# Performance work log

Hardware: AMD Instinct MI355X
Metric: run time of the kernel (lower is better)

Reference implementation:

```python
import jax, jax.numpy as jnp
import numpy as np

NUM_HEADS = 16


def setup_inputs() -> dict:
    key = jax.random.key(0)
    k1, k2, k3 = jax.random.split(key, 3)
    T, B, E = 2048, 2, 1024
    query = jax.random.normal(k1, (T, B, E), dtype=jnp.float32)
    # xavier-uniform-ish init for qkv weight, small normal for output proj
    lim = (6.0 / (3 * E + E)) ** 0.5
    W_qkv = jax.random.uniform(k2, (3 * E, E), dtype=jnp.float32, minval=-lim, maxval=lim)
    W_o = jax.random.normal(k3, (E, E), dtype=jnp.float32) * 0.02
    b_qkv = jnp.zeros((3 * E,), dtype=jnp.float32)
    b_o = jnp.zeros((E,), dtype=jnp.float32)
    return {"query": query, "W_qkv": W_qkv, "b_qkv": b_qkv, "W_o": W_o, "b_o": b_o}


def reference(query, W_qkv, b_qkv, W_o, b_o):
    T, B, E = query.shape
    H = NUM_HEADS
    hd = E // H
    scaling = float(hd) ** -0.5

    # fused qkv projection: [T, B, 3E]
    qkv = jnp.einsum('tbe,fe->tbf', query, W_qkv) + b_qkv
    q, k, v = jnp.split(qkv, 3, axis=-1)
    q = q * scaling

    def to_heads(x):  # [T, B, E] -> [B*H, T, hd]
        return x.reshape(T, B * H, hd).transpose(1, 0, 2)

    q, k, v = to_heads(q), to_heads(k), to_heads(v)

    # explicit bmm QK^T -> softmax -> bmm AV (faithful to source)
    scores = jnp.einsum('bqd,bkd->bqk', q, k)          # [B*H, T, T]
    attn = jax.nn.softmax(scores, axis=-1)             # dropout p=0.0 (eval)
    ctx = jnp.einsum('bqk,bkd->bqd', attn, v)          # [B*H, T, hd]

    out = ctx.transpose(1, 0, 2).reshape(T, B, E)
    out = jnp.einsum('tbe,fe->tbf', out, W_o) + b_o    # o_net

    avg_weights = attn.reshape(B, H, T, T).sum(axis=1) / H  # need_weights=True path
    return out, avg_weights
```

## Files before the change

kernel.cpp:

```cpp
#include <hip/hip_runtime.h>
#include <stdint.h>

typedef unsigned short u16;
typedef __bf16 bf16x8 __attribute__((ext_vector_type(8)));
typedef float f32x4 __attribute__((ext_vector_type(4)));
typedef float f32x16 __attribute__((ext_vector_type(16)));

__device__ __forceinline__ u16 f2b(float f) {
  unsigned u = __builtin_bit_cast(unsigned, f);
  u += 0x7fffu + ((u >> 16) & 1u);
  return (u16)(u >> 16);
}

__device__ __forceinline__ float fexp2(float x) { return __builtin_amdgcn_exp2f(x); }

__device__ __forceinline__ void gld_lds16(const void* g, void* l) {
  __builtin_amdgcn_global_load_lds((const __attribute__((address_space(1))) unsigned int*)g,
                                   (__attribute__((address_space(3))) unsigned int*)l,
                                   16, 0, 0);
}

__global__ __launch_bounds__(256) void k_cvt3(
    const float* __restrict__ s0, u16* __restrict__ d0,
    const float* __restrict__ s1, u16* __restrict__ d1,
    const float* __restrict__ s2, u16* __restrict__ d2) {
  const int bx = blockIdx.x;
  const float* s;
  u16* d;
  int i0;
  if (bx < 4096)      { s = s0; d = d0; i0 = bx; }
  else if (bx < 7168) { s = s1; d = d1; i0 = bx - 4096; }
  else                { s = s2; d = d2; i0 = bx - 7168; }
  const int i = i0 * 256 + threadIdx.x;
  float4 v = reinterpret_cast<const float4*>(s)[i];
  ushort4 o;
  o.x = f2b(v.x); o.y = f2b(v.y); o.z = f2b(v.z); o.w = f2b(v.w);
  reinterpret_cast<ushort4*>(d)[i] = o;
}

template <int EPI>
__device__ __forceinline__ void gemm_body(
    const u16* __restrict__ A, const u16* __restrict__ B, const float* __restrict__ bias,
    float* __restrict__ outF, u16* __restrict__ q_ws, u16* __restrict__ k_ws,
    u16* __restrict__ vt_ws, int tm, int tn, u16* smem) {
  u16* Al0 = smem;
  u16* Bl0 = smem + 8192;
  const int tid = threadIdx.x;
  const int w = tid >> 6, lane = tid & 63;
  const int wr = w >> 1, wc = w & 1;
  const int lo = lane & 15, hi = lane >> 4;
  const size_t arow0 = (size_t)tm * 128;
  const size_t brow0 = (size_t)tn * 128;

  f32x4 acc[4][4] = {};

  const int rr = lane >> 2;
  const int kswz = ((lane & 3) ^ ((rr >> 1) & 3)) * 8;
  const int rsw = (lo >> 1) & 3;

  for (int rs = 0; rs < 2; ++rs) {
    int seg = rs * 4 + w;
    gld_lds16(A + (arow0 + seg * 16 + rr) * 1024 + kswz, &Al0[seg * 512 + lane * 8]);
    gld_lds16(B + (brow0 + seg * 16 + rr) * 1024 + kswz, &Bl0[seg * 512 + lane * 8]);
  }
  __syncthreads();
  int cur = 0;
  for (int kb = 0; kb < 32; ++kb) {
    if (kb + 1 < 32) {
      const int k0 = (kb + 1) * 32 + kswz;
      u16* Ad = Al0 + (cur ^ 1) * 4096;
      u16* Bd = Bl0 + (cur ^ 1) * 4096;
      for (int rs = 0; rs < 2; ++rs) {
        int seg = rs * 4 + w;
        gld_lds16(A + (arow0 + seg * 16 + rr) * 1024 + k0, &Ad[seg * 512 + lane * 8]);
        gld_lds16(B + (brow0 + seg * 16 + rr) * 1024 + k0, &Bd[seg * 512 + lane * 8]);
      }
    }
    const u16* Ac = Al0 + cur * 4096;
    const u16* Bc = Bl0 + cur * 4096;
    bf16x8 af[4], bfr[4];
#pragma unroll
    for (int m = 0; m < 4; ++m)
      af[m] = *(const bf16x8*)&Ac[(wr * 64 + m * 16 + lo) * 32 + ((hi ^ rsw) * 8)];
#pragma unroll
    for (int n = 0; n < 4; ++n)
      bfr[n] = *(const bf16x8*)&Bc[(wc * 64 + n * 16 + lo) * 32 + ((hi ^ rsw) * 8)];
#pragma unroll
    for (int m = 0; m < 4; ++m)
#pragma unroll
      for (int n = 0; n < 4; ++n)
        acc[m][n] = __builtin_amdgcn_mfma_f32_16x16x32_bf16(af[m], bfr[n], acc[m][n], 0, 0, 0);
    __syncthreads();
    cur ^= 1;
  }

  if (EPI == 0) {
#pragma unroll
    for (int n = 0; n < 4; ++n) {
      const int col = tn * 128 + wc * 64 + n * 16 + lo;
      const float bb = bias[col];
#pragma unroll
      for (int m = 0; m < 4; ++m)
#pragma unroll
        for (int r = 0; r < 4; ++r) {
          const int row = tm * 128 + wr * 64 + m * 16 + hi * 4 + r;
          outF[(size_t)row * 1024 + col] = acc[m][n][r] + bb;
        }
    }
  } else {
    const int sec = tn >> 3;
#pragma unroll
    for (int n = 0; n < 4; ++n) {
      const int cin = (tn & 7) * 128 + wc * 64 + n * 16 + lo;
      const int h = cin >> 6, d = cin & 63;
      const float bb = bias[sec * 1024 + cin];
#pragma unroll
      for (int m = 0; m < 4; ++m) {
        const int rowb = tm * 128 + wr * 64 + m * 16 + hi * 4;
        const int t0 = rowb >> 1;
        const float v0 = acc[m][n][0] + bb, v1 = acc[m][n][1] + bb;
        const float v2 = acc[m][n][2] + bb, v3 = acc[m][n][3] + bb;
        if (sec == 0) {
          const float s = 0.18033688f;
          q_ws[(((size_t)h * 2048 + t0) * 64) + d]            = f2b(v0 * s);
          q_ws[(((size_t)(16 + h) * 2048 + t0) * 64) + d]     = f2b(v1 * s);
          q_ws[(((size_t)h * 2048 + t0 + 1) * 64) + d]        = f2b(v2 * s);
          q_ws[(((size_t)(16 + h) * 2048 + t0 + 1) * 64) + d] = f2b(v3 * s);
        } else if (sec == 1) {
          k_ws[(((size_t)h * 2048 + t0) * 64) + d]            = f2b(v0);
          k_ws[(((size_t)(16 + h) * 2048 + t0) * 64) + d]     = f2b(v1);
          k_ws[(((size_t)h * 2048 + t0 + 1) * 64) + d]        = f2b(v2);
          k_ws[(((size_t)(16 + h) * 2048 + t0 + 1) * 64) + d] = f2b(v3);
        } else {
          const int tp0 = (t0 & ~12) | ((t0 & 4) << 1) | ((t0 & 8) >> 1);
          ushort2 p0, p1;
          p0.x = f2b(v0); p0.y = f2b(v2);
          p1.x = f2b(v1); p1.y = f2b(v3);
          *(ushort2*)(vt_ws + ((size_t)h * 64 + d) * 2048 + tp0) = p0;
          *(ushort2*)(vt_ws + ((size_t)(16 + h) * 64 + d) * 2048 + tp0) = p1;
        }
      }
    }
  }
}

__global__ __launch_bounds__(256) void k_gemm_qkv(
    const u16* __restrict__ A, const u16* __restrict__ B, const float* __restrict__ bias,
    u16* __restrict__ q_ws, u16* __restrict__ k_ws, u16* __restrict__ vt_ws) {
  __shared__ __align__(16) u16 smem[16384];
  gemm_body<1>(A, B, bias, nullptr, q_ws, k_ws, vt_ws, blockIdx.y, blockIdx.x, smem);
}

__global__ __launch_bounds__(256) void k_gemm_out(
    const u16* __restrict__ ctx, const u16* __restrict__ wobf, const float* __restrict__ bo,
    float* __restrict__ out) {
  __shared__ __align__(16) u16 smem[16384];
  gemm_body<0>(ctx, wobf, bo, out, nullptr, nullptr, nullptr, blockIdx.y, blockIdx.x, smem);
}

__global__ __launch_bounds__(1024) void k_flash(
    const u16* __restrict__ q_ws, const u16* __restrict__ k_ws, const u16* __restrict__ vt_ws,
    u16* __restrict__ ctx_ws, float* __restrict__ c_ws) {
  __shared__ __align__(16) u16 KVl[33792];
  const int tid = threadIdx.x, w = tid >> 6, lane = tid & 63;
  const int h = lane >> 5, l31 = lane & 31, l7 = lane & 7;
  const int hh = w >> 3;
  const int wq = w & 7;
  const int tid_h = tid & 511;

  const int flat = blockIdx.y * 8 + blockIdx.x;
  const int xcd = flat & 7, idx = flat >> 3;
  const int bh = xcd * 4 + (idx & 3);
  const int qtile = idx >> 2;
  const int b = bh >> 4, head = bh & 15;
  const int qbase = qtile * 256;
  const int qrow = qbase + wq * 32 + l31;

  bf16x8 qf[4];
#pragma unroll
  for (int j = 0; j < 4; ++j)
    qf[j] = *(const bf16x8*)(q_ws + ((size_t)bh * 2048 + qrow) * 64 + j * 16 + h * 8);

  const int srow = tid_h >> 3, schk = tid_h & 7;
  const int xc = (schk ^ (srow & 7)) * 8;
  const u16* kgA = k_ws + ((size_t)bh * 2048 + hh * 1024 + srow) * 64 + xc;
  const u16* vgA = vt_ws + ((size_t)bh * 64 + srow) * 2048 + hh * 1024 + xc;

  f32x16 ca0 = {}, ca1 = {};
  float lrow = 0.f;

  {
    u16* base = KVl + hh * 8192;
    gld_lds16(kgA, base + tid_h * 8);
    gld_lds16(vgA, base + 4096 + tid_h * 8);
  }
  __syncthreads();

  int cur = 0;
  for (int it = 0; it < 16; ++it) {
    if (it < 15) {
      u16* base = KVl + (cur ^ 1) * 16384 + hh * 8192;
      gld_lds16(kgA + (size_t)(it + 1) * 4096, base + tid_h * 8);
      gld_lds16(vgA + (it + 1) * 64, base + 4096 + tid_h * 8);
    }
    const char* Kb = (const char*)(KVl + cur * 16384 + hh * 8192);
    const char* Vb = Kb + 8192;

    f32x16 st0 = {}, st1 = {};
    __builtin_amdgcn_s_setprio(1);
#pragma unroll
    for (int j = 0; j < 4; ++j) {
      bf16x8 k0 = *(const bf16x8*)(Kb + l31 * 128 + (((2 * j + h) ^ l7) * 16));
      bf16x8 k1 = *(const bf16x8*)(Kb + (32 + l31) * 128 + (((2 * j + h) ^ l7) * 16));
      st0 = __builtin_amdgcn_mfma_f32_32x32x16_bf16(k0, qf[j], st0, 0, 0, 0);
      st1 = __builtin_amdgcn_mfma_f32_32x32x16_bf16(k1, qf[j], st1, 0, 0, 0);
    }
    __builtin_amdgcn_s_setprio(0);

    float ps0 = 0.f, ps1 = 0.f;
#pragma unroll
    for (int r = 0; r < 16; ++r) { float p = fexp2(st0[r]); st0[r] = p; ps0 += p; }
#pragma unroll
    for (int r = 0; r < 16; ++r) { float p = fexp2(st1[r]); st1[r] = p; ps1 += p; }
    float ps = ps0 + ps1;
    ps += __shfl_xor(ps, 32, 64);
    lrow += ps;

    bf16x8 pb00, pb01, pb10, pb11;
#pragma unroll
    for (int i = 0; i < 8; ++i) {
      pb00[i] = (__bf16)st0[i];
      pb01[i] = (__bf16)st0[8 + i];
      pb10[i] = (__bf16)st1[i];
      pb11[i] = (__bf16)st1[8 + i];
    }

    __builtin_amdgcn_s_setprio(1);
#pragma unroll
    for (int t2 = 0; t2 < 2; ++t2)
#pragma unroll
      for (int kp = 0; kp < 2; ++kp) {
        const int ch = (4 * t2 + 2 * kp + h) ^ l7;
        bf16x8 v0 = *(const bf16x8*)(Vb + l31 * 128 + ch * 16);
        bf16x8 v1 = *(const bf16x8*)(Vb + (32 + l31) * 128 + ch * 16);
        const bf16x8 pv = (t2 == 0) ? (kp == 0 ? pb00 : pb01) : (kp == 0 ? pb10 : pb11);
        ca0 = __builtin_amdgcn_mfma_f32_32x32x16_bf16(v0, pv, ca0, 0, 0, 0);
        ca1 = __builtin_amdgcn_mfma_f32_32x32x16_bf16(v1, pv, ca1, 0, 0, 0);
      }
    __builtin_amdgcn_s_setprio(0);

    __syncthreads();
    cur ^= 1;
  }

  float* F = (float*)KVl;
  if (w >= 8) {
    const int g = w - 8;
#pragma unroll
    for (int r = 0; r < 16; ++r) {
      F[g * 2048 + r * 64 + lane] = ca0[r];
      F[g * 2048 + (16 + r) * 64 + lane] = ca1[r];
    }
    F[16384 + g * 64 + lane] = lrow;
  }
  __syncthreads();
  float inv = 0.f;
  if (w < 8) {
#pragma unroll
    for (int r = 0; r < 16; ++r) {
      ca0[r] += F[w * 2048 + r * 64 + lane];
      ca1[r] += F[w * 2048 + (16 + r) * 64 + lane];
    }
    lrow += F[16384 + w * 64 + lane];
    inv = 1.0f / lrow;
    if (lane < 32) c_ws[(size_t)bh * 2048 + qrow] = inv;
  }
  __syncthreads();
  u16* tw = KVl + w * 2048;
  if (w < 8) {
#pragma unroll
    for (int r = 0; r < 16; ++r) {
      const int d0 = (r & 3) + 8 * (r >> 2) + 4 * h;
      const int d1 = 32 + d0;
      *(u16*)((char*)tw + l31 * 128 + ((2 * d0) ^ (l7 << 4))) = f2b(ca0[r] * inv);
      *(u16*)((char*)tw + l31 * 128 + ((2 * d1) ^ (l7 << 4))) = f2b(ca1[r] * inv);
    }
  }
  __syncthreads();
  if (w < 8) {
#pragma unroll
    for (int it = 0; it < 4; ++it) {
      const int row = it * 8 + (lane >> 3);
      uint4 val = *(const uint4*)((const char*)tw + row * 128 + (((lane & 7) ^ (row & 7)) * 16));
      const int q = qbase + wq * 32 + row;
      *(uint4*)(ctx_ws + ((size_t)(q * 2 + b)) * 1024 + head * 64 + (lane & 7) * 8) = val;
    }
  }
}

__global__ __launch_bounds__(256) void k_avg(
    const u16* __restrict__ q_ws, const u16* __restrict__ k_ws,
    const float* __restrict__ c_ws, float* __restrict__ avg) {
  __shared__ __align__(16) u16 Kl[2][4096];
  const int tid = threadIdx.x, w = tid >> 6, lane = tid & 63;
  const int lo = lane & 15, hi = lane >> 4;
  const int kbase = blockIdx.x * 64;
  const int qb = blockIdx.y * 64;
  const int b = blockIdx.z;
  const int qrow = qb + w * 16 + lo;
  const int qrow_base = qb + w * 16 + hi * 4;

  const int r0 = tid >> 3, c0 = tid & 7;
  const int ldsoff = r0 * 128 + ((c0 ^ (r0 & 7)) << 4);
  const u16* kg = k_ws + ((size_t)(b * 16) * 2048 + kbase + r0) * 64 + c0 * 8;
  const int l7 = lo & 7;

  float acc[4][4] = {};
  const f32x4 zero = {0.f, 0.f, 0.f, 0.f};

  uint4 rg0 = *(const uint4*)(kg);
  uint4 rg1 = *(const uint4*)(kg + 32 * 64);
  {
    char* dst = (char*)Kl[0] + ldsoff;
    *(uint4*)(dst) = rg0;
    *(uint4*)(dst + 32 * 128) = rg1;
  }
  __syncthreads();

  int cur = 0;
  for (int h = 0; h < 16; ++h) {
    const int bh = b * 16 + h;
    if (h + 1 < 16) {
      const u16* kgn = kg + (size_t)(h + 1) * 2048 * 64;
      rg0 = *(const uint4*)(kgn);
      rg1 = *(const uint4*)(kgn + 32 * 64);
    }
    const u16* qp = q_ws + ((size_t)bh * 2048 + qrow) * 64 + hi * 8;
    bf16x8 qf0 = *(const bf16x8*)qp;
    bf16x8 qf1 = *(const bf16x8*)(qp + 32);
    const float4 cf = *(const float4*)(c_ws + (size_t)bh * 2048 + qrow_base);
    const float cfa[4] = {cf.x, cf.y, cf.z, cf.w};
    const char* kbse = (const char*)Kl[cur];
#pragma unroll
    for (int n = 0; n < 4; ++n) {
      const char* kp = kbse + (n * 16 + lo) * 128;
      bf16x8 k0 = *(const bf16x8*)(kp + ((hi ^ l7) << 4));
      bf16x8 k1 = *(const bf16x8*)(kp + (((hi + 4) ^ l7) << 4));
      f32x4 s = __builtin_amdgcn_mfma_f32_16x16x32_bf16(qf0, k0, zero, 0, 0, 0);
      s = __builtin_amdgcn_mfma_f32_16x16x32_bf16(qf1, k1, s, 0, 0, 0);
#pragma unroll
      for (int r = 0; r < 4; ++r) acc[n][r] += fexp2(s[r]) * cfa[r];
    }
    if (h + 1 < 16) {
      char* dst = (char*)Kl[cur ^ 1] + ldsoff;
      *(uint4*)(dst) = rg0;
      *(uint4*)(dst + 32 * 128) = rg1;
      __syncthreads();
    }
    cur ^= 1;
  }

  const float s16 = 1.0f / 16.0f;
#pragma unroll
  for (int n = 0; n < 4; ++n)
#pragma unroll
    for (int r = 0; r < 4; ++r)
      avg[((size_t)(b * 2048 + qrow_base + r)) * 2048 + kbase + n * 16 + lo] = acc[n][r] * s16;
}

extern "C" void kernel_launch(void* const* d_in, const int* in_sizes, int n_in,
                              void* d_out, int out_size, void* d_ws, size_t ws_size,
                              hipStream_t stream) {
  const float* query = (const float*)d_in[0];
  const float* Wqkv  = (const float*)d_in[1];
  const float* bqkv  = (const float*)d_in[2];
  const float* Wo    = (const float*)d_in[3];
  const float* bo    = (const float*)d_in[4];
  float* out = (float*)d_out;
  float* avg = out + (size_t)4096 * 1024;

  char* ws = (char*)d_ws;
  u16* qbf    = (u16*)(ws);
  u16* ctx_ws = (u16*)(ws);
  u16*   wqkvbf = (u16*)(ws + 8388608);
  float* c_ws   = (float*)(ws + 8388608);
  u16* wobf  = (u16*)(ws + 14680064);
  u16* q_ws  = (u16*)(ws + 16777216);
  u16* k_ws  = (u16*)(ws + 25165824);
  u16* vt_ws = (u16*)(ws + 33554432);

  k_cvt3<<<dim3(8192), dim3(256), 0, stream>>>(query, qbf, Wqkv, wqkvbf, Wo, wobf);
  k_gemm_qkv<<<dim3(24, 32), dim3(256), 0, stream>>>(
      qbf, wqkvbf, bqkv, q_ws, k_ws, vt_ws);
  k_flash<<<dim3(8, 32), dim3(1024), 0, stream>>>(
      q_ws, k_ws, vt_ws, ctx_ws, c_ws);
  k_avg<<<dim3(32, 32, 2), dim3(256), 0, stream>>>(
      q_ws, k_ws, c_ws, avg);
  k_gemm_out<<<dim3(8, 32), dim3(256), 0, stream>>>(
      ctx_ws, wobf, bo, out);
}
```

Measured before the change: 166.3 us.

## Merge avg-weights and output GEMM into one launch, widen avg tiles, remap QKV blocks

Replaces the separate k_avg and k_gemm_out launches with a single k_tail kernel. Its first 256 blocks do the output projection and the remaining 1024 blocks compute the head-averaged attention weights. The avg tile widens from 64 to 128 keys per block, so each block reuses Q fragments and c_ws across twice the keys at the cost of more accumulator registers. The QKV GEMM also remaps block indices so consecutive tiles go to the same XCD, aiming for better L2 locality. Together these cut one launch gap, let the two independent tail workloads overlap, and halve redundant Q loads in the avg pass.

Result: faster. 140.0 us (-15.8%).

```diff
diff --git a/kernel.cpp b/kernel.cpp
--- a/kernel.cpp
+++ b/kernel.cpp
@@ -148,14 +148,102 @@
     const u16* __restrict__ A, const u16* __restrict__ B, const float* __restrict__ bias,
     u16* __restrict__ q_ws, u16* __restrict__ k_ws, u16* __restrict__ vt_ws) {
   __shared__ __align__(16) u16 smem[16384];
-  gemm_body<1>(A, B, bias, nullptr, q_ws, k_ws, vt_ws, blockIdx.y, blockIdx.x, smem);
-}
-
-__global__ __launch_bounds__(256) void k_gemm_out(
+  const int flat = blockIdx.y * 24 + blockIdx.x;
+  const int xcd = flat & 7, idx = flat >> 3;
+  const int wg = xcd * 96 + idx;
+  gemm_body<1>(A, B, bias, nullptr, q_ws, k_ws, vt_ws, wg / 24, wg % 24, smem);
+}
+
+__device__ __forceinline__ void avg_body(
+    const u16* __restrict__ q_ws, const u16* __restrict__ k_ws,
+    const float* __restrict__ c_ws, float* __restrict__ avg,
+    int kx, int qy, int b, u16* smem) {
+  u16* Kl0 = smem;
+  const int tid = threadIdx.x, w = tid >> 6, lane = tid & 63;
+  const int lo = lane & 15, hi = lane >> 4;
+  const int kbase = kx * 128;
+  const int qb = qy * 64;
+  const int qrow = qb + w * 16 + lo;
+  const int qrow_base = qb + w * 16 + hi * 4;
+
+  const int r0 = tid >> 3, c0 = tid & 7;
+  const int ldsoff = r0 * 128 + ((c0 ^ (r0 & 7)) << 4);
+  const u16* kg = k_ws + ((size_t)(b * 16) * 2048 + kbase + r0) * 64 + c0 * 8;
+  const int l7 = lo & 7;
+
+  float acc[8][4] = {};
+  const f32x4 zero = {0.f, 0.f, 0.f, 0.f};
+
+  uint4 rg0 = *(const uint4*)(kg);
+  uint4 rg1 = *(const uint4*)(kg + 32 * 64);
+  uint4 rg2 = *(const uint4*)(kg + 64 * 64);
+  uint4 rg3 = *(const uint4*)(kg + 96 * 64);
+  {
+    char* dst = (char*)Kl0 + ldsoff;
+    *(uint4*)(dst) = rg0;
+    *(uint4*)(dst + 32 * 128) = rg1;
+    *(uint4*)(dst + 64 * 128) = rg2;
+    *(uint4*)(dst + 96 * 128) = rg3;
+  }
+  __syncthreads();
+
+  int cur = 0;
+  for (int h = 0; h < 16; ++h) {
+    const int bh = b * 16 + h;
+    if (h + 1 < 16) {
+      const u16* kgn = kg + (size_t)(h + 1) * 2048 * 64;
+      rg0 = *(const uint4*)(kgn);
+      rg1 = *(const uint4*)(kgn + 32 * 64);
+      rg2 = *(const uint4*)(kgn + 64 * 64);
+      rg3 = *(const uint4*)(kgn + 96 * 64);
+    }
+    const u16* qp = q_ws + ((size_t)bh * 2048 + qrow) * 64 + hi * 8;
+    bf16x8 qf0 = *(const bf16x8*)qp;
+    bf16x8 qf1 = *(const bf16x8*)(qp + 32);
+    const float4 cf = *(const float4*)(c_ws + (size_t)bh * 2048 + qrow_base);
+    const float cfa[4] = {cf.x, cf.y, cf.z, cf.w};
+    const char* kbse = (const char*)(Kl0 + cur * 8192);
+#pragma unroll
+    for (int n = 0; n < 8; ++n) {
+      const char* kp = kbse + (n * 16 + lo) * 128;
+      bf16x8 k0 = *(const bf16x8*)(kp + ((hi ^ l7) << 4));
+      bf16x8 k1 = *(const bf16x8*)(kp + (((hi + 4) ^ l7) << 4));
+      f32x4 s = __builtin_amdgcn_mfma_f32_16x16x32_bf16(qf0, k0, zero, 0, 0, 0);
+      s = __builtin_amdgcn_mfma_f32_16x16x32_bf16(qf1, k1, s, 0, 0, 0);
+#pragma unroll
+      for (int r = 0; r < 4; ++r) acc[n][r] += fexp2(s[r]) * cfa[r];
+    }
+    if (h + 1 < 16) {
+      char* dst = (char*)(Kl0 + (cur ^ 1) * 8192) + ldsoff;
+      *(uint4*)(dst) = rg0;
+      *(uint4*)(dst + 32 * 128) = rg1;
+      *(uint4*)(dst + 64 * 128) = rg2;
+      *(uint4*)(dst + 96 * 128) = rg3;
+      __syncthreads();
+    }
+    cur ^= 1;
+  }
+
+  const float s16 = 1.0f / 16.0f;
+#pragma unroll
+  for (int n = 0; n < 8; ++n)
+#pragma unroll
+    for (int r = 0; r < 4; ++r)
+      avg[((size_t)(b * 2048 + qrow_base + r)) * 2048 + kbase + n * 16 + lo] = acc[n][r] * s16;
+}
+
+__global__ __launch_bounds__(256) void k_tail(
     const u16* __restrict__ ctx, const u16* __restrict__ wobf, const float* __restrict__ bo,
-    float* __restrict__ out) {
+    float* __restrict__ out, const u16* __restrict__ q_ws, const u16* __restrict__ k_ws,
+    const float* __restrict__ c_ws, float* __restrict__ avg) {
   __shared__ __align__(16) u16 smem[16384];
-  gemm_body<0>(ctx, wobf, bo, out, nullptr, nullptr, nullptr, blockIdx.y, blockIdx.x, smem);
+  const int bx = blockIdx.x;
+  if (bx < 256) {
+    gemm_body<0>(ctx, wobf, bo, out, nullptr, nullptr, nullptr, bx >> 3, bx & 7, smem);
+  } else {
+    const int id = bx - 256;
+    avg_body(q_ws, k_ws, c_ws, avg, id & 15, (id >> 4) & 31, id >> 9, smem);
+  }
 }
 
 __global__ __launch_bounds__(1024) void k_flash(
@@ -296,76 +384,6 @@
       *(uint4*)(ctx_ws + ((size_t)(q * 2 + b)) * 1024 + head * 64 + (lane & 7) * 8) = val;
     }
   }
-}
-
-__global__ __launch_bounds__(256) void k_avg(
-    const u16* __restrict__ q_ws, const u16* __restrict__ k_ws,
-    const float* __restrict__ c_ws, float* __restrict__ avg) {
-  __shared__ __align__(16) u16 Kl[2][4096];
-  const int tid = threadIdx.x, w = tid >> 6, lane = tid & 63;
-  const int lo = lane & 15, hi = lane >> 4;
-  const int kbase = blockIdx.x * 64;
-  const int qb = blockIdx.y * 64;
-  const int b = blockIdx.z;
-  const int qrow = qb + w * 16 + lo;
-  const int qrow_base = qb + w * 16 + hi * 4;
-
-  const int r0 = tid >> 3, c0 = tid & 7;
-  const int ldsoff = r0 * 128 + ((c0 ^ (r0 & 7)) << 4);
-  const u16* kg = k_ws + ((size_t)(b * 16) * 2048 + kbase + r0) * 64 + c0 * 8;
-  const int l7 = lo & 7;
-
-  float acc[4][4] = {};
-  const f32x4 zero = {0.f, 0.f, 0.f, 0.f};
-
-  uint4 rg0 = *(const uint4*)(kg);
-  uint4 rg1 = *(const uint4*)(kg + 32 * 64);
-  {
-    char* dst = (char*)Kl[0] + ldsoff;
-    *(uint4*)(dst) = rg0;
-    *(uint4*)(dst + 32 * 128) = rg1;
-  }
-  __syncthreads();
-
-  int cur = 0;
-  for (int h = 0; h < 16; ++h) {
-    const int bh = b * 16 + h;
-    if (h + 1 < 16) {
-      const u16* kgn = kg + (size_t)(h + 1) * 2048 * 64;
-      rg0 = *(const uint4*)(kgn);
-      rg1 = *(const uint4*)(kgn + 32 * 64);
-    }
-    const u16* qp = q_ws + ((size_t)bh * 2048 + qrow) * 64 + hi * 8;
-    bf16x8 qf0 = *(const bf16x8*)qp;
-    bf16x8 qf1 = *(const bf16x8*)(qp + 32);
-    const float4 cf = *(const float4*)(c_ws + (size_t)bh * 2048 + qrow_base);
-    const float cfa[4] = {cf.x, cf.y, cf.z, cf.w};
-    const char* kbse = (const char*)Kl[cur];
-#pragma unroll
-    for (int n = 0; n < 4; ++n) {
-      const char* kp = kbse + (n * 16 + lo) * 128;
-      bf16x8 k0 = *(const bf16x8*)(kp + ((hi ^ l7) << 4));
-      bf16x8 k1 = *(const bf16x8*)(kp + (((hi + 4) ^ l7) << 4));
-      f32x4 s = __builtin_amdgcn_mfma_f32_16x16x32_bf16(qf0, k0, zero, 0, 0, 0);
-      s = __builtin_amdgcn_mfma_f32_16x16x32_bf16(qf1, k1, s, 0, 0, 0);
-#pragma unroll
-      for (int r = 0; r < 4; ++r) acc[n][r] += fexp2(s[r]) * cfa[r];
-    }
-    if (h + 1 < 16) {
-      char* dst = (char*)Kl[cur ^ 1] + ldsoff;
-      *(uint4*)(dst) = rg0;
-      *(uint4*)(dst + 32 * 128) = rg1;
-      __syncthreads();
-    }
-    cur ^= 1;
-  }
-
-  const float s16 = 1.0f / 16.0f;
-#pragma unroll
-  for (int n = 0; n < 4; ++n)
-#pragma unroll
-    for (int r = 0; r < 4; ++r)
-      avg[((size_t)(b * 2048 + qrow_base + r)) * 2048 + kbase + n * 16 + lo] = acc[n][r] * s16;
 }
 
 extern "C" void kernel_launch(void* const* d_in, const int* in_sizes, int n_in,
@@ -394,8 +412,6 @@
       qbf, wqkvbf, bqkv, q_ws, k_ws, vt_ws);
   k_flash<<<dim3(8, 32), dim3(1024), 0, stream>>>(
       q_ws, k_ws, vt_ws, ctx_ws, c_ws);
-  k_avg<<<dim3(32, 32, 2), dim3(256), 0, stream>>>(
-      q_ws, k_ws, c_ws, avg);
-  k_gemm_out<<<dim3(8, 32), dim3(256), 0, stream>>>(
-      ctx_ws, wobf, bo, out);
-}
+  k_tail<<<dim3(1280), dim3(256), 0, stream>>>(
+      ctx_ws, wobf, bo, out, q_ws, k_ws, c_ws, avg);
+}
```
